# Performance work log

Measured on AMD Instinct MI355X. Metric: run time of the kernel, lower is better.

The kernel has to match this reference:

```python
import jax, jax.numpy as jnp
import numpy as np

S, B, D, H, K, M, MEM = 1024, 2, 1024, 16, 64, 4096, 1
T = (MEM + 1) * S  # key length = (mem_len+1)*seq_len


def setup_inputs() -> dict:
    key = jax.random.key(0)
    ks = jax.random.split(key, 16)

    def w(k, shape):  # N(0, 0.02) init as in the torch module
        return jax.random.normal(k, shape, dtype=jnp.float32) * 0.02

    x = jax.random.normal(ks[0], (S, B, D), dtype=jnp.float32)
    p = jax.random.normal(ks[1], (T, B, D), dtype=jnp.float32)
    memory = jax.random.normal(ks[2], (MEM * S, B, D), dtype=jnp.float32)
    u_bias = w(ks[3], (H, K))
    v_bias = w(ks[4], (H, K))
    # Transformer-XL causal mask: query s may attend to keys t <= mem_len*S + s
    t_idx = jnp.arange(T)[None, :]
    s_idx = jnp.arange(S)[:, None]
    mask = jnp.where(t_idx <= MEM * S + s_idx, 0.0, -1e9).astype(jnp.float32)[None]  # [1,S,T]
    return {
        "x": x, "p": p, "mask": mask, "memory": memory,
        "u_bias": u_bias, "v_bias": v_bias,
        "wq_w": w(ks[5], (H * K, D)), "wke_w": w(ks[6], (H * K, D)),
        "wkr_w": w(ks[7], (H * K, D)), "wv_w": w(ks[8], (H * K, D)),
        "wc_w": w(ks[9], (D, H * K)),
        "w1_w": w(ks[10], (M, D)), "w1_b": jnp.zeros((M,), jnp.float32),
        "w2_w": w(ks[11], (D, M)), "w2_b": jnp.zeros((D,), jnp.float32),
        "ln1_g": jnp.ones((D,), jnp.float32), "ln1_b": jnp.zeros((D,), jnp.float32),
        "ln2_g": jnp.ones((D,), jnp.float32), "ln2_b": jnp.zeros((D,), jnp.float32),
    }


def _layernorm(x, g, b, eps=1e-5):
    mu = jnp.mean(x, axis=-1, keepdims=True)
    var = jnp.mean(jnp.square(x - mu), axis=-1, keepdims=True)
    return (x - mu) / jnp.sqrt(var + eps) * g + b


def reference(x, p, mask, memory, u_bias, v_bias,
              wq_w, wke_w, wkr_w, wv_w, wc_w,
              w1_w, w1_b, w2_w, w2_b, ln1_g, ln1_b, ln2_g, ln2_b):
    s_len, b_sz, d = x.shape
    q = (x @ wq_w.T).reshape(s_len, b_sz, H, K)            # [S,B,H,K]
    x_mem = jnp.concatenate([memory, x], axis=0)           # [T,B,D]
    k_e = (x_mem @ wke_w.T).reshape(T, b_sz, H, K)         # content keys
    k_r = (p @ wkr_w.T).reshape(T, b_sz, H, K)             # relative-position keys
    v = (x_mem @ wv_w.T).reshape(T, b_sz, H, K)
    # AC: content score, BD: relative-position score (Transformer-XL)
    ac = jnp.einsum("sbhk,tbhk->bhst", q + u_bias, k_e)
    bd = jnp.einsum("sbhk,tbhk->bhst", q + v_bias, k_r)
    alpha = (ac + bd) / np.sqrt(K).astype(np.float32) + mask[:, None]  # [B,H,S,T]
    alpha = jax.nn.softmax(alpha, axis=-1)
    av = jnp.einsum("bhst,tbhk->sbhk", alpha, v).reshape(s_len, b_sz, H * K)
    u = av @ wc_w.T
    u = _layernorm(u + x, ln1_g, ln1_b)
    z = jax.nn.relu(u @ w1_w.T + w1_b) @ w2_w.T + w2_b
    z = _layernorm(z + u, ln2_g, ln2_b)
    return z
```

## Files before the change

kernel.cpp:

```cpp
#include <hip/hip_runtime.h>
#include <math.h>

#define S_LEN 1024
#define BATCH 2
#define DM 1024
#define NH 16
#define HD 64
#define FFN_DIM 4096
#define T_LEN 2048
#define RQ 2048
#define RT 4096
#define KROW 72
#define NPART 3
#define OPSTR 2097152L

typedef __attribute__((ext_vector_type(8))) short short8;
typedef __attribute__((ext_vector_type(4))) float f32x4;

__device__ __forceinline__ unsigned short f2bf(float f) {
    unsigned u = __builtin_bit_cast(unsigned, f);
    u += 0x7fffu + ((u >> 16) & 1u);
    return (unsigned short)(u >> 16);
}
__device__ __forceinline__ float bf2f(unsigned short s) { return __builtin_bit_cast(float, ((unsigned)s) << 16); }

#define GLD_LDS16(gptr, lptr)                                                                  \
    __builtin_amdgcn_global_load_lds((const __attribute__((address_space(1))) unsigned int*)(gptr), \
                                     (__attribute__((address_space(3))) unsigned int*)(lptr), 16, 0, 0)

__device__ __forceinline__ ushort4 cvt4(float4 v) {
    ushort4 o;
    o.x = f2bf(v.x); o.y = f2bf(v.y); o.z = f2bf(v.z); o.w = f2bf(v.w);
    return o;
}

__global__ void cast_all_kernel(const float* __restrict__ wq, const float* __restrict__ wke,
                                const float* __restrict__ wv, const float* __restrict__ wkr,
                                const float* __restrict__ wc, const float* __restrict__ w1,
                                const float* __restrict__ w2, const float* __restrict__ x,
                                const float* __restrict__ p, const float* __restrict__ mem,
                                unsigned short* __restrict__ wdst, unsigned short* __restrict__ xbf,
                                unsigned short* __restrict__ pbf, unsigned short* __restrict__ xm) {
    const long Q = 256 * 1024;
    const long W = 13 * Q;
    long i = (long)blockIdx.x * blockDim.x + threadIdx.x;
    if (i < W) {
        const float* src; long off;
        if      (i < 1 * Q) { src = wq;  off = 0; }
        else if (i < 2 * Q) { src = wke; off = 1 * Q; }
        else if (i < 3 * Q) { src = wv;  off = 2 * Q; }
        else if (i < 4 * Q) { src = wkr; off = 3 * Q; }
        else if (i < 5 * Q) { src = wc;  off = 4 * Q; }
        else if (i < 9 * Q) { src = w1;  off = 5 * Q; }
        else                { src = w2;  off = 9 * Q; }
        ((ushort4*)wdst)[i] = cvt4(((const float4*)src)[i - off]);
    } else if (i < W + 2 * Q) {
        long j = i - W;
        ((ushort4*)xbf)[j] = cvt4(((const float4*)x)[j]);
    } else if (i < W + 6 * Q) {
        long j = i - W - 2 * Q;
        ((ushort4*)pbf)[j] = cvt4(((const float4*)p)[j]);
    } else {
        long j = i - W - 6 * Q;
        float4 v = (j < 2 * Q) ? ((const float4*)mem)[j] : ((const float4*)x)[j - 2 * Q];
        ((ushort4*)xm)[j] = cvt4(v);
    }
}

#define BM 128
#define BN 128
#define BK 64


__launch_bounds__(256)
__global__ void proj_fused(const unsigned short* __restrict__ xbf, const unsigned short* __restrict__ xmbf,
                           const unsigned short* __restrict__ pbf, const unsigned short* __restrict__ wqb,
                           const unsigned short* __restrict__ wkevb, const unsigned short* __restrict__ wkrb,
                           unsigned short* __restrict__ qo, unsigned short* __restrict__ keo,
                           unsigned short* __restrict__ vTo, unsigned short* __restrict__ kro) {
    __shared__ __align__(16) short As[BM * BK];
    __shared__ __align__(16) short Bs[BN * BK];
    const int id = blockIdx.x;
    const unsigned short *A, *B;
    unsigned short *Yb, *Yv = nullptr;
    int bx, by;
    if (id < 128)      { A = xbf;  B = wqb;   Yb = qo;  bx = id & 7;   by = id >> 3; }
    else if (id < 640) { int t = id - 128; A = xmbf; B = wkevb; Yb = keo; Yv = vTo;
                         bx = t & 15; by = t >> 4; }
    else               { int t = id - 640; A = pbf;  B = wkrb;  Yb = kro;
                         bx = t & 7;  by = t >> 3; }
    const int tid = threadIdx.x;
    const int w = tid >> 6, lane = tid & 63;
    const int row0 = by * BM, col0 = bx * BN;
    const int wr = (w >> 1) * 64, wcn = (w & 1) * 64;
    f32x4 acc[4][4] = {};
    const int lrow = lane & 15, quad = lane >> 4;
    for (int k0 = 0; k0 < DM; k0 += BK) {
        __syncthreads();
#pragma unroll
        for (int i = 0; i < 4; ++i) {
            int c = i * 256 + tid;
            int row = c >> 3, ph = c & 7;
            int kl = (ph - row) & 7;
            GLD_LDS16(A + (long)(row0 + row) * DM + k0 + kl * 8, As + (i * 256 + w * 64) * 8);
            GLD_LDS16(B + (long)(col0 + row) * DM + k0 + kl * 8, Bs + (i * 256 + w * 64) * 8);
        }
        __syncthreads();
#pragma unroll
        for (int hh = 0; hh < 2; ++hh) {
            short8 a[4], b[4];
#pragma unroll
            for (int mi = 0; mi < 4; ++mi) {
                int r = wr + mi * 16 + lrow;
                int ph = (hh * 4 + quad + r) & 7;
                a[mi] = *(const short8*)&As[r * BK + ph * 8];
            }
#pragma unroll
            for (int ni = 0; ni < 4; ++ni) {
                int r = wcn + ni * 16 + lrow;
                int ph = (hh * 4 + quad + r) & 7;
                b[ni] = *(const short8*)&Bs[r * BK + ph * 8];
            }
#pragma unroll
            for (int mi = 0; mi < 4; ++mi)
#pragma unroll
                for (int ni = 0; ni < 4; ++ni)
                    acc[mi][ni] = __builtin_amdgcn_mfma_f32_16x16x32_bf16(a[mi], b[ni], acc[mi][ni], 0, 0, 0);
        }
    }
    const int mb = row0 + wr + quad * 4;
    const int nb = col0 + wcn + lrow;
    const bool isv = (Yv != nullptr) && (col0 >= 1024);
#pragma unroll
    for (int mi = 0; mi < 4; ++mi)
#pragma unroll
        for (int ni = 0; ni < 4; ++ni) {
            const int r = mb + mi * 16, cc = nb + ni * 16;
#pragma unroll
            for (int reg = 0; reg < 4; ++reg) {
                float val = acc[mi][ni][reg];
                const int rf = r + reg;
                if (isv) {
                    int c2 = cc - 1024;
                    int t = rf >> 1, b2 = rf & 1;
                    int h2 = c2 >> 6, d2 = c2 & 63;
                    Yv[((long)(b2 * NH + h2) * HD + d2) * T_LEN + t] = f2bf(val);
                } else {
                    Yb[(long)rf * DM + cc] = f2bf(val);
                }
            }
        }
}

__launch_bounds__(256)
__global__ void gemm_mfma(const unsigned short* __restrict__ A, const unsigned short* __restrict__ B,
                          const float* __restrict__ bias, float* __restrict__ Yf,
                          unsigned short* __restrict__ Yb, int Kd, int N, int relu,
                          int klen, long pstride) {
    __shared__ __align__(16) short As[BM * BK];
    __shared__ __align__(16) short Bs[BN * BK];
    const int tid = threadIdx.x;
    const int w = tid >> 6, lane = tid & 63;
    const int row0 = blockIdx.y * BM, col0 = blockIdx.x * BN;
    const int kbeg = blockIdx.z * klen;
    const int wr = (w >> 1) * 64, wcn = (w & 1) * 64;
    f32x4 acc[4][4] = {};
    const int lrow = lane & 15, quad = lane >> 4;
    for (int k0 = kbeg; k0 < kbeg + klen; k0 += BK) {
        __syncthreads();
#pragma unroll
        for (int i = 0; i < 4; ++i) {
            int c = i * 256 + tid;
            int row = c >> 3, ph = c & 7;
            int kl = (ph - row) & 7;
            GLD_LDS16(A + (long)(row0 + row) * Kd + k0 + kl * 8, As + (i * 256 + w * 64) * 8);
            GLD_LDS16(B + (long)(col0 + row) * Kd + k0 + kl * 8, Bs + (i * 256 + w * 64) * 8);
        }
        __syncthreads();
#pragma unroll
        for (int hh = 0; hh < 2; ++hh) {
            short8 a[4], b[4];
#pragma unroll
            for (int mi = 0; mi < 4; ++mi) {
                int r = wr + mi * 16 + lrow;
                int ph = (hh * 4 + quad + r) & 7;
                a[mi] = *(const short8*)&As[r * BK + ph * 8];
            }
#pragma unroll
            for (int ni = 0; ni < 4; ++ni) {
                int r = wcn + ni * 16 + lrow;
                int ph = (hh * 4 + quad + r) & 7;
                b[ni] = *(const short8*)&Bs[r * BK + ph * 8];
            }
#pragma unroll
            for (int mi = 0; mi < 4; ++mi)
#pragma unroll
                for (int ni = 0; ni < 4; ++ni)
                    acc[mi][ni] = __builtin_amdgcn_mfma_f32_16x16x32_bf16(a[mi], b[ni], acc[mi][ni], 0, 0, 0);
        }
    }
    const int mb = row0 + wr + quad * 4;
    const int nb = col0 + wcn + lrow;
    float* of = Yf ? Yf + (long)blockIdx.z * pstride : nullptr;
    float bb[4];
#pragma unroll
    for (int ni = 0; ni < 4; ++ni) bb[ni] = bias ? bias[nb + ni * 16] : 0.f;
#pragma unroll
    for (int mi = 0; mi < 4; ++mi)
#pragma unroll
        for (int ni = 0; ni < 4; ++ni) {
            const int r = mb + mi * 16, cc = nb + ni * 16;
#pragma unroll
            for (int reg = 0; reg < 4; ++reg) {
                float val = acc[mi][ni][reg] + bb[ni];
                if (relu) val = fmaxf(val, 0.f);
                if (Yb) Yb[(long)(r + reg) * N + cc] = f2bf(val);
                else    of[(long)(r + reg) * N + cc] = val;
            }
        }
}

__launch_bounds__(256)
__global__ void prep_kernel(const unsigned short* __restrict__ kr,
                            const float* __restrict__ ub, const float* __restrict__ vb,
                            unsigned short* __restrict__ ke_io, float* __restrict__ biasg) {
    const int r = blockIdx.x;
    const int tid = threadIdx.x;
    const int h = tid >> 4, seg = tid & 15;
    ushort4 keu = ((const ushort4*)(ke_io + (long)r * DM))[tid];
    ushort4 kru = ((const ushort4*)(kr + (long)r * DM))[tid];
    float ke0 = bf2f(keu.x), ke1 = bf2f(keu.y), ke2 = bf2f(keu.z), ke3 = bf2f(keu.w);
    float kr0 = bf2f(kru.x), kr1 = bf2f(kru.y), kr2 = bf2f(kru.z), kr3 = bf2f(kru.w);
    float4 u4 = ((const float4*)ub)[tid];
    float4 v4 = ((const float4*)vb)[tid];
    ushort4 s;
    s.x = f2bf((ke0 + kr0) * 0.125f); s.y = f2bf((ke1 + kr1) * 0.125f);
    s.z = f2bf((ke2 + kr2) * 0.125f); s.w = f2bf((ke3 + kr3) * 0.125f);
    ((ushort4*)(ke_io + (long)r * DM))[tid] = s;
    float part = u4.x * ke0 + u4.y * ke1 + u4.z * ke2 + u4.w * ke3
               + v4.x * kr0 + v4.y * kr1 + v4.z * kr2 + v4.w * kr3;
    part += __shfl_xor(part, 1);
    part += __shfl_xor(part, 2);
    part += __shfl_xor(part, 4);
    part += __shfl_xor(part, 8);
    if (seg == 0) {
        const int t = r >> 1, b = r & 1;
        biasg[(b * NH + h) * T_LEN + t] = part * 0.125f;
    }
}

__launch_bounds__(256)
__global__ void attn_mfma(const unsigned short* __restrict__ qg,
                          const unsigned short* __restrict__ ksum,
                          const unsigned short* __restrict__ vT,
                          const float* __restrict__ biasg,
                          float* __restrict__ Op01, float* __restrict__ Op2,
                          float2* __restrict__ mlout) {
    __shared__ __align__(16) unsigned short Ks[64 * KROW];
    __shared__ __align__(16) unsigned short Vs[64 * KROW];
    __shared__ __align__(16) unsigned short Ps[4][16 * KROW];
    const int bid = blockIdx.x;
    const int part = bid >> 9, rid = bid & 511;
    const int stile = rid & 15, h = (rid >> 4) & 15, b = rid >> 8;
    const int tid = threadIdx.x, w = tid >> 6, lane = tid & 63;
    const int L = lane & 15, quad = lane >> 4;
    const int qbase = stile * 64 + w * 16;
    short8 qf0, qf1;
    {
        const unsigned short* qp = qg + ((long)(qbase + L) * 2 + b) * DM + h * HD + quad * 8;
        qf0 = *(const short8*)(qp);
        qf1 = *(const short8*)(qp + 32);
    }
    f32x4 O[4] = {};
    float mrow[4] = {-1e30f, -1e30f, -1e30f, -1e30f};
    float lrow[4] = {0.f, 0.f, 0.f, 0.f};
    const int nch = 17 + stile;
    const float* bias_p = biasg + (long)(b * NH + h) * T_LEN;
    const unsigned short* ks_base = ksum + (long)b * DM + h * HD;
    const unsigned short* vt_base = vT + (long)(b * NH + h) * HD * T_LEN;
    const int c0 = tid, c1 = 256 + tid;
    const int row_a = c0 >> 3, seg_a = c0 & 7;
    const int row_b = c1 >> 3, seg_b = c1 & 7;
    uint4 pk0, pk1, pv0, pv1;
    float pb[4];
    {
        const int tf = part * 64;
        pk0 = *(const uint4*)(ks_base + (long)(tf + row_a) * 2 * DM + seg_a * 8);
        pk1 = *(const uint4*)(ks_base + (long)(tf + row_b) * 2 * DM + seg_b * 8);
        pv0 = *(const uint4*)(vt_base + (long)row_a * T_LEN + tf + seg_a * 8);
        pv1 = *(const uint4*)(vt_base + (long)row_b * T_LEN + tf + seg_b * 8);
#pragma unroll
        for (int kt = 0; kt < 4; ++kt) pb[kt] = bias_p[tf + kt * 16 + L];
    }
    for (int ch = part; ch < nch; ch += NPART) {
        const int t0 = ch * 64;
        __syncthreads();
        *(uint4*)&Ks[row_a * KROW + seg_a * 8] = pk0;
        *(uint4*)&Ks[row_b * KROW + seg_b * 8] = pk1;
        *(uint4*)&Vs[row_a * KROW + seg_a * 8] = pv0;
        *(uint4*)&Vs[row_b * KROW + seg_b * 8] = pv1;
        __syncthreads();
        const bool more = (ch + NPART < nch);
        float pbn[4];
        if (more) {
            const int t1 = t0 + NPART * 64;
            pk0 = *(const uint4*)(ks_base + (long)(t1 + row_a) * 2 * DM + seg_a * 8);
            pk1 = *(const uint4*)(ks_base + (long)(t1 + row_b) * 2 * DM + seg_b * 8);
            pv0 = *(const uint4*)(vt_base + (long)row_a * T_LEN + t1 + seg_a * 8);
            pv1 = *(const uint4*)(vt_base + (long)row_b * T_LEN + t1 + seg_b * 8);
#pragma unroll
            for (int kt = 0; kt < 4; ++kt) pbn[kt] = bias_p[t1 + kt * 16 + L];
        }
        f32x4 S[4] = {};
#pragma unroll
        for (int kt = 0; kt < 4; ++kt) {
            short8 kb0 = *(const short8*)&Ks[(kt * 16 + L) * KROW + quad * 8];
            short8 kb1 = *(const short8*)&Ks[(kt * 16 + L) * KROW + 32 + quad * 8];
            S[kt] = __builtin_amdgcn_mfma_f32_16x16x32_bf16(qf0, kb0, S[kt], 0, 0, 0);
            S[kt] = __builtin_amdgcn_mfma_f32_16x16x32_bf16(qf1, kb1, S[kt], 0, 0, 0);
        }
        float sc[4][4];
        float cm[4] = {-1e30f, -1e30f, -1e30f, -1e30f};
        if (ch != nch - 1) {
#pragma unroll
            for (int kt = 0; kt < 4; ++kt)
#pragma unroll
                for (int reg = 0; reg < 4; ++reg) {
                    float v = S[kt][reg] + pb[kt];
                    sc[kt][reg] = v;
                    cm[reg] = fmaxf(cm[reg], v);
                }
        } else {
#pragma unroll
            for (int kt = 0; kt < 4; ++kt)
#pragma unroll
                for (int reg = 0; reg < 4; ++reg) {
                    float v = S[kt][reg] + pb[kt];
                    if (t0 + kt * 16 + L > 1024 + qbase + quad * 4 + reg) v = -1e30f;
                    sc[kt][reg] = v;
                    cm[reg] = fmaxf(cm[reg], v);
                }
        }
#pragma unroll
        for (int off = 1; off < 16; off <<= 1)
#pragma unroll
            for (int reg = 0; reg < 4; ++reg) cm[reg] = fmaxf(cm[reg], __shfl_xor(cm[reg], off));
        float cf[4];
#pragma unroll
        for (int reg = 0; reg < 4; ++reg) {
            float mn = fmaxf(mrow[reg], cm[reg]);
            cf[reg] = __expf(mrow[reg] - mn);
            mrow[reg] = mn;
            lrow[reg] *= cf[reg];
        }
        float rs[4] = {0.f, 0.f, 0.f, 0.f};
#pragma unroll
        for (int kt = 0; kt < 4; ++kt)
#pragma unroll
            for (int reg = 0; reg < 4; ++reg) {
                float pv = __expf(sc[kt][reg] - mrow[reg]);
                rs[reg] += pv;
                Ps[w][(quad * 4 + reg) * KROW + kt * 16 + L] = f2bf(pv);
            }
#pragma unroll
        for (int off = 1; off < 16; off <<= 1)
#pragma unroll
            for (int reg = 0; reg < 4; ++reg) rs[reg] += __shfl_xor(rs[reg], off);
#pragma unroll
        for (int reg = 0; reg < 4; ++reg) lrow[reg] += rs[reg];
#pragma unroll
        for (int dt = 0; dt < 4; ++dt)
#pragma unroll
            for (int reg = 0; reg < 4; ++reg) O[dt][reg] *= cf[reg];
        short8 pa0 = *(const short8*)&Ps[w][L * KROW + quad * 8];
        short8 pa1 = *(const short8*)&Ps[w][L * KROW + 32 + quad * 8];
#pragma unroll
        for (int dt = 0; dt < 4; ++dt) {
            short8 vb0 = *(const short8*)&Vs[(dt * 16 + L) * KROW + quad * 8];
            short8 vb1 = *(const short8*)&Vs[(dt * 16 + L) * KROW + 32 + quad * 8];
            O[dt] = __builtin_amdgcn_mfma_f32_16x16x32_bf16(pa0, vb0, O[dt], 0, 0, 0);
            O[dt] = __builtin_amdgcn_mfma_f32_16x16x32_bf16(pa1, vb1, O[dt], 0, 0, 0);
        }
        if (more) {
#pragma unroll
            for (int kt = 0; kt < 4; ++kt) pb[kt] = pbn[kt];
        }
    }
    float* ob = (part < 2) ? Op01 + (long)part * OPSTR : Op2;
    const long rbase = ((long)b * NH + h) * S_LEN;
#pragma unroll
    for (int reg = 0; reg < 4; ++reg) {
        const int s = qbase + quad * 4 + reg;
        float* op = ob + (rbase + s) * 64;
#pragma unroll
        for (int dt = 0; dt < 4; ++dt) op[dt * 16 + L] = O[dt][reg];
        if (L == 0) mlout[(long)part * 32768 + rbase + s] = make_float2(mrow[reg], lrow[reg]);
    }
}

__launch_bounds__(256)
__global__ void attn_combine(const float* __restrict__ Op01, const float* __restrict__ Op2,
                             const float2* __restrict__ ml,
                             unsigned short* __restrict__ avout) {
    const int i = blockIdx.x * 256 + threadIdx.x;
    const int d4 = i & 15;
    const int row = i >> 4;
    const int s = row & 1023;
    const int bh = row >> 10;
    const int b = bh >> 4, h = bh & 15;
    float2 m0 = ml[row], m1 = ml[row + 32768], m2 = ml[row + 65536];
    float m = fmaxf(fmaxf(m0.x, m1.x), m2.x);
    float a0 = __expf(m0.x - m), a1 = __expf(m1.x - m), a2 = __expf(m2.x - m);
    float inv = 1.f / (a0 * m0.y + a1 * m1.y + a2 * m2.y);
    a0 *= inv; a1 *= inv; a2 *= inv;
    float4 o0 = ((const float4*)Op01)[(long)row * 16 + d4];
    float4 o1 = ((const float4*)Op01)[((long)row + 32768) * 16 + d4];
    float4 o2 = ((const float4*)Op2)[(long)row * 16 + d4];
    float4 o;
    o.x = a0 * o0.x + a1 * o1.x + a2 * o2.x;
    o.y = a0 * o0.y + a1 * o1.y + a2 * o2.y;
    o.z = a0 * o0.z + a1 * o1.z + a2 * o2.z;
    o.w = a0 * o0.w + a1 * o1.w + a2 * o2.w;
    *(ushort4*)(avout + ((long)s * 2 + b) * DM + h * HD + d4 * 4) = cvt4(o);
}

__launch_bounds__(256)
__global__ void ln_kernel(const float* __restrict__ a0, const float* __restrict__ a1,
                          const float* __restrict__ cb, const float* __restrict__ r,
                          const float* __restrict__ g, const float* __restrict__ be,
                          float* __restrict__ out, unsigned short* __restrict__ outb) {
    const int row = blockIdx.x;
    const int tid = threadIdx.x;
    float4 xa = ((const float4*)(a0 + (long)row * DM))[tid];
    if (a1) {
        float4 x1 = ((const float4*)(a1 + (long)row * DM))[tid];
        xa.x += x1.x; xa.y += x1.y; xa.z += x1.z; xa.w += x1.w;
    }
    if (cb) {
        float4 c4 = ((const float4*)cb)[tid];
        xa.x += c4.x; xa.y += c4.y; xa.z += c4.z; xa.w += c4.w;
    }
    float4 xr = ((const float4*)(r + (long)row * DM))[tid];
    float4 x = make_float4(xa.x + xr.x, xa.y + xr.y, xa.z + xr.z, xa.w + xr.w);
    float s1 = x.x + x.y + x.z + x.w;
    float s2 = x.x * x.x + x.y * x.y + x.z * x.z + x.w * x.w;
#pragma unroll
    for (int off = 32; off > 0; off >>= 1) {
        s1 += __shfl_down(s1, off);
        s2 += __shfl_down(s2, off);
    }
    __shared__ float w1s[4], w2s[4];
    const int wid = tid >> 6;
    if ((tid & 63) == 0) { w1s[wid] = s1; w2s[wid] = s2; }
    __syncthreads();
    float S1 = w1s[0] + w1s[1] + w1s[2] + w1s[3];
    float S2 = w2s[0] + w2s[1] + w2s[2] + w2s[3];
    float mu = S1 * (1.f / 1024.f);
    float var = S2 * (1.f / 1024.f) - mu * mu;
    float rstd = rsqrtf(var + 1e-5f);
    float4 gv = ((const float4*)g)[tid];
    float4 bv = ((const float4*)be)[tid];
    float4 o;
    o.x = (x.x - mu) * rstd * gv.x + bv.x;
    o.y = (x.y - mu) * rstd * gv.y + bv.y;
    o.z = (x.z - mu) * rstd * gv.z + bv.z;
    o.w = (x.w - mu) * rstd * gv.w + bv.w;
    ((float4*)(out + (long)row * DM))[tid] = o;
    if (outb) ((ushort4*)(outb + (long)row * DM))[tid] = cvt4(o);
}

extern "C" void kernel_launch(void* const* d_in, const int* in_sizes, int n_in,
                              void* d_out, int out_size, void* d_ws, size_t ws_size,
                              hipStream_t stream) {
    (void)in_sizes; (void)n_in; (void)out_size; (void)ws_size;
    const float* x    = (const float*)d_in[0];
    const float* p    = (const float*)d_in[1];
    const float* mem  = (const float*)d_in[3];
    const float* ub   = (const float*)d_in[4];
    const float* vb   = (const float*)d_in[5];
    const float* wq   = (const float*)d_in[6];
    const float* wke  = (const float*)d_in[7];
    const float* wkr  = (const float*)d_in[8];
    const float* wv   = (const float*)d_in[9];
    const float* wc   = (const float*)d_in[10];
    const float* w1   = (const float*)d_in[11];
    const float* w1b  = (const float*)d_in[12];
    const float* w2   = (const float*)d_in[13];
    const float* w2b  = (const float*)d_in[14];
    const float* ln1g = (const float*)d_in[15];
    const float* ln1b = (const float*)d_in[16];
    const float* ln2g = (const float*)d_in[17];
    const float* ln2b = (const float*)d_in[18];
    float* out = (float*)d_out;
    float* wsf = (float*)d_ws;
    unsigned short* ws16 = (unsigned short*)d_ws;

    const long HLF = 512 * 1024;
    const long M16 = 1024 * 1024;
    unsigned short* wq_bf   = ws16 + 0 * M16;
    unsigned short* wkev_bf = ws16 + 1 * M16;
    unsigned short* wkr_bf  = ws16 + 3 * M16;
    unsigned short* wc_bf   = ws16 + 4 * M16;
    unsigned short* w1_bf   = ws16 + 5 * M16;
    unsigned short* w2_bf   = ws16 + 9 * M16;
    unsigned short* x_bf   = (unsigned short*)(wsf + 13 * HLF);
    unsigned short* xm_bf  = (unsigned short*)(wsf + 15 * HLF);
    unsigned short* p_bf   = (unsigned short*)(wsf + 19 * HLF);
    unsigned short* q_bf   = (unsigned short*)(wsf + 23 * HLF);
    unsigned short* ke_bf  = (unsigned short*)(wsf + 25 * HLF);
    unsigned short* kr_bf  = (unsigned short*)(wsf + 29 * HLF);
    unsigned short* vT_bf  = (unsigned short*)(wsf + 33 * HLF);
    float* abias           = wsf + 37 * HLF;
    float2* mlpart         = (float2*)(wsf + 13 * HLF);
    float* Op01            = wsf + 15 * HLF;
    float* Op2             = wsf + 29 * HLF;
    unsigned short* avb_bf = (unsigned short*)(wsf + 33 * HLF);
    float* t1p             = wsf + 15 * HLF;
    float* u               = wsf + 25 * HLF;
    unsigned short* u_bf   = (unsigned short*)(wsf + 23 * HLF);
    unsigned short* z1_bf  = (unsigned short*)(wsf + 13 * HLF);
    float* t2p             = wsf + 29 * HLF;
    const long PSTR = (long)2048 * 1024;

    cast_all_kernel<<<23552, 256, 0, stream>>>(wq, wke, wv, wkr, wc, w1, w2, x, p, mem,
                                               ws16, x_bf, p_bf, xm_bf);
    proj_fused<<<896, 256, 0, stream>>>(x_bf, xm_bf, p_bf, wq_bf, wkev_bf, wkr_bf,
                                        q_bf, ke_bf, vT_bf, kr_bf);
    prep_kernel<<<RT, 256, 0, stream>>>(kr_bf, ub, vb, ke_bf, abias);
    attn_mfma<<<512 * NPART, 256, 0, stream>>>(q_bf, ke_bf, vT_bf, abias, Op01, Op2, mlpart);
    attn_combine<<<2048, 256, 0, stream>>>(Op01, Op2, mlpart, avb_bf);
    gemm_mfma<<<dim3(8, 16, 2), 256, 0, stream>>>(avb_bf, wc_bf, nullptr, t1p, nullptr,
                                                  DM, DM, 0, 512, PSTR);
    ln_kernel<<<RQ, 256, 0, stream>>>(t1p, t1p + PSTR, nullptr, x, ln1g, ln1b, u, u_bf);
    gemm_mfma<<<dim3(32, 16, 1), 256, 0, stream>>>(u_bf, w1_bf, w1b, nullptr, z1_bf,
                                                   DM, FFN_DIM, 1, DM, 0);
    gemm_mfma<<<dim3(8, 16, 2), 256, 0, stream>>>(z1_bf, w2_bf, nullptr, t2p, nullptr,
                                                  FFN_DIM, DM, 0, 2048, PSTR);
    ln_kernel<<<RQ, 256, 0, stream>>>(t2p, t2p + PSTR, w2b, u, ln2g, ln2b, out, nullptr);
}
```

Baseline: 381.8 us.

## Remap blocks across XCDs, halve projection K-tile, add MFMA priority hints

Block indices in the projection, attention and GEMM kernels are permuted so that consecutive logical tiles land on the same XCD (the index is taken modulo 8 and strided), which should improve L2 reuse of shared operand panels. The GEMM launches become 1D grids whose tile coordinates are decoded in-kernel. The fused projection kernel's K-tile drops from 64 to 32 with a new LDS swizzle, halving its LDS footprint to allow more resident blocks, at the cost of twice as many barriers. The attention kernel wraps its MFMA sections in s_setprio so the matrix work gets issue priority over other waves.

```diff
diff --git a/kernel.cpp b/kernel.cpp
--- a/kernel.cpp
+++ b/kernel.cpp
@@ -7,9 +7,9 @@
 #define NH 16
 #define HD 64
 #define FFN_DIM 4096
-#define T_LEN 2048
 #define RQ 2048
 #define RT 4096
+#define T_LEN 2048
 #define KROW 72
 #define NPART 3
 #define OPSTR 2097152L
@@ -69,8 +69,8 @@
 
 #define BM 128
 #define BN 128
-#define BK 64
-
+#define GBK 64
+#define PBK 32
 
 __launch_bounds__(256)
 __global__ void proj_fused(const unsigned short* __restrict__ xbf, const unsigned short* __restrict__ xmbf,
@@ -78,9 +78,10 @@
                            const unsigned short* __restrict__ wkevb, const unsigned short* __restrict__ wkrb,
                            unsigned short* __restrict__ qo, unsigned short* __restrict__ keo,
                            unsigned short* __restrict__ vTo, unsigned short* __restrict__ kro) {
-    __shared__ __align__(16) short As[BM * BK];
-    __shared__ __align__(16) short Bs[BN * BK];
-    const int id = blockIdx.x;
+    __shared__ __align__(16) short As[BM * PBK];
+    __shared__ __align__(16) short Bs[BN * PBK];
+    const int id0 = blockIdx.x;
+    const int id = (id0 & 7) * 112 + (id0 >> 3);
     const unsigned short *A, *B;
     unsigned short *Yb, *Yv = nullptr;
     int bx, by;
@@ -95,38 +96,35 @@
     const int wr = (w >> 1) * 64, wcn = (w & 1) * 64;
     f32x4 acc[4][4] = {};
     const int lrow = lane & 15, quad = lane >> 4;
-    for (int k0 = 0; k0 < DM; k0 += BK) {
+    for (int k0 = 0; k0 < DM; k0 += PBK) {
         __syncthreads();
 #pragma unroll
-        for (int i = 0; i < 4; ++i) {
-            int c = i * 256 + tid;
-            int row = c >> 3, ph = c & 7;
-            int kl = (ph - row) & 7;
-            GLD_LDS16(A + (long)(row0 + row) * DM + k0 + kl * 8, As + (i * 256 + w * 64) * 8);
-            GLD_LDS16(B + (long)(col0 + row) * DM + k0 + kl * 8, Bs + (i * 256 + w * 64) * 8);
+        for (int i = 0; i < 2; ++i) {
+            int c = w * 128 + i * 64 + lane;
+            int row = c >> 2, kg = c & 3;
+            int kl = (kg - (row >> 1)) & 3;
+            GLD_LDS16(A + (long)(row0 + row) * DM + k0 + kl * 8, As + (w * 128 + i * 64) * 8);
+            GLD_LDS16(B + (long)(col0 + row) * DM + k0 + kl * 8, Bs + (w * 128 + i * 64) * 8);
         }
         __syncthreads();
-#pragma unroll
-        for (int hh = 0; hh < 2; ++hh) {
-            short8 a[4], b[4];
-#pragma unroll
-            for (int mi = 0; mi < 4; ++mi) {
-                int r = wr + mi * 16 + lrow;
-                int ph = (hh * 4 + quad + r) & 7;
-                a[mi] = *(const short8*)&As[r * BK + ph * 8];
-            }
-#pragma unroll
-            for (int ni = 0; ni < 4; ++ni) {
-                int r = wcn + ni * 16 + lrow;
-                int ph = (hh * 4 + quad + r) & 7;
-                b[ni] = *(const short8*)&Bs[r * BK + ph * 8];
-            }
-#pragma unroll
-            for (int mi = 0; mi < 4; ++mi)
-#pragma unroll
-                for (int ni = 0; ni < 4; ++ni)
-                    acc[mi][ni] = __builtin_amdgcn_mfma_f32_16x16x32_bf16(a[mi], b[ni], acc[mi][ni], 0, 0, 0);
-        }
+        short8 a[4], b[4];
+#pragma unroll
+        for (int mi = 0; mi < 4; ++mi) {
+            int r = wr + mi * 16 + lrow;
+            int ph = (quad + (r >> 1)) & 3;
+            a[mi] = *(const short8*)&As[r * PBK + ph * 8];
+        }
+#pragma unroll
+        for (int ni = 0; ni < 4; ++ni) {
+            int r = wcn + ni * 16 + lrow;
+            int ph = (quad + (r >> 1)) & 3;
+            b[ni] = *(const short8*)&Bs[r * PBK + ph * 8];
+        }
+#pragma unroll
+        for (int mi = 0; mi < 4; ++mi)
+#pragma unroll
+            for (int ni = 0; ni < 4; ++ni)
+                acc[mi][ni] = __builtin_amdgcn_mfma_f32_16x16x32_bf16(a[mi], b[ni], acc[mi][ni], 0, 0, 0);
     }
     const int mb = row0 + wr + quad * 4;
     const int nb = col0 + wcn + lrow;
@@ -157,16 +155,23 @@
                           const float* __restrict__ bias, float* __restrict__ Yf,
                           unsigned short* __restrict__ Yb, int Kd, int N, int relu,
                           int klen, long pstride) {
-    __shared__ __align__(16) short As[BM * BK];
-    __shared__ __align__(16) short Bs[BN * BK];
+    __shared__ __align__(16) short As[BM * GBK];
+    __shared__ __align__(16) short Bs[BN * GBK];
+    const int nbx = N >> 7;
+    const int cpx = gridDim.x >> 3;
+    const int bid = ((blockIdx.x & 7) * cpx) + (blockIdx.x >> 3);
+    const int per_z = nbx << 4;
+    const int z = bid / per_z;
+    const int r2 = bid - z * per_z;
+    const int by = r2 / nbx, bx = r2 - by * nbx;
     const int tid = threadIdx.x;
     const int w = tid >> 6, lane = tid & 63;
-    const int row0 = blockIdx.y * BM, col0 = blockIdx.x * BN;
-    const int kbeg = blockIdx.z * klen;
+    const int row0 = by * BM, col0 = bx * BN;
+    const int kbeg = z * klen;
     const int wr = (w >> 1) * 64, wcn = (w & 1) * 64;
     f32x4 acc[4][4] = {};
     const int lrow = lane & 15, quad = lane >> 4;
-    for (int k0 = kbeg; k0 < kbeg + klen; k0 += BK) {
+    for (int k0 = kbeg; k0 < kbeg + klen; k0 += GBK) {
         __syncthreads();
 #pragma unroll
         for (int i = 0; i < 4; ++i) {
@@ -184,13 +189,13 @@
             for (int mi = 0; mi < 4; ++mi) {
                 int r = wr + mi * 16 + lrow;
                 int ph = (hh * 4 + quad + r) & 7;
-                a[mi] = *(const short8*)&As[r * BK + ph * 8];
+                a[mi] = *(const short8*)&As[r * GBK + ph * 8];
             }
 #pragma unroll
             for (int ni = 0; ni < 4; ++ni) {
                 int r = wcn + ni * 16 + lrow;
                 int ph = (hh * 4 + quad + r) & 7;
-                b[ni] = *(const short8*)&Bs[r * BK + ph * 8];
+                b[ni] = *(const short8*)&Bs[r * GBK + ph * 8];
             }
 #pragma unroll
             for (int mi = 0; mi < 4; ++mi)
@@ -201,7 +206,7 @@
     }
     const int mb = row0 + wr + quad * 4;
     const int nb = col0 + wcn + lrow;
-    float* of = Yf ? Yf + (long)blockIdx.z * pstride : nullptr;
+    float* of = Yf ? Yf + (long)z * pstride : nullptr;
     float bb[4];
 #pragma unroll
     for (int ni = 0; ni < 4; ++ni) bb[ni] = bias ? bias[nb + ni * 16] : 0.f;
@@ -259,7 +264,8 @@
     __shared__ __align__(16) unsigned short Ks[64 * KROW];
     __shared__ __align__(16) unsigned short Vs[64 * KROW];
     __shared__ __align__(16) unsigned short Ps[4][16 * KROW];
-    const int bid = blockIdx.x;
+    const int bid0 = blockIdx.x;
+    const int bid = (bid0 & 7) * 192 + (bid0 >> 3);
     const int part = bid >> 9, rid = bid & 511;
     const int stile = rid & 15, h = (rid >> 4) & 15, b = rid >> 8;
     const int tid = threadIdx.x, w = tid >> 6, lane = tid & 63;
@@ -312,6 +318,7 @@
             for (int kt = 0; kt < 4; ++kt) pbn[kt] = bias_p[t1 + kt * 16 + L];
         }
         f32x4 S[4] = {};
+        __builtin_amdgcn_s_setprio(1);
 #pragma unroll
         for (int kt = 0; kt < 4; ++kt) {
             short8 kb0 = *(const short8*)&Ks[(kt * 16 + L) * KROW + quad * 8];
@@ -319,6 +326,7 @@
             S[kt] = __builtin_amdgcn_mfma_f32_16x16x32_bf16(qf0, kb0, S[kt], 0, 0, 0);
             S[kt] = __builtin_amdgcn_mfma_f32_16x16x32_bf16(qf1, kb1, S[kt], 0, 0, 0);
         }
+        __builtin_amdgcn_s_setprio(0);
         float sc[4][4];
         float cm[4] = {-1e30f, -1e30f, -1e30f, -1e30f};
         if (ch != nch - 1) {
@@ -374,6 +382,7 @@
             for (int reg = 0; reg < 4; ++reg) O[dt][reg] *= cf[reg];
         short8 pa0 = *(const short8*)&Ps[w][L * KROW + quad * 8];
         short8 pa1 = *(const short8*)&Ps[w][L * KROW + 32 + quad * 8];
+        __builtin_amdgcn_s_setprio(1);
 #pragma unroll
         for (int dt = 0; dt < 4; ++dt) {
             short8 vb0 = *(const short8*)&Vs[(dt * 16 + L) * KROW + quad * 8];
@@ -381,6 +390,7 @@
             O[dt] = __builtin_amdgcn_mfma_f32_16x16x32_bf16(pa0, vb0, O[dt], 0, 0, 0);
             O[dt] = __builtin_amdgcn_mfma_f32_16x16x32_bf16(pa1, vb1, O[dt], 0, 0, 0);
         }
+        __builtin_amdgcn_s_setprio(0);
         if (more) {
 #pragma unroll
             for (int kt = 0; kt < 4; ++kt) pb[kt] = pbn[kt];
@@ -529,12 +539,12 @@
     prep_kernel<<<RT, 256, 0, stream>>>(kr_bf, ub, vb, ke_bf, abias);
     attn_mfma<<<512 * NPART, 256, 0, stream>>>(q_bf, ke_bf, vT_bf, abias, Op01, Op2, mlpart);
     attn_combine<<<2048, 256, 0, stream>>>(Op01, Op2, mlpart, avb_bf);
-    gemm_mfma<<<dim3(8, 16, 2), 256, 0, stream>>>(avb_bf, wc_bf, nullptr, t1p, nullptr,
-                                                  DM, DM, 0, 512, PSTR);
+    gemm_mfma<<<256, 256, 0, stream>>>(avb_bf, wc_bf, nullptr, t1p, nullptr,
+                                       DM, DM, 0, 512, PSTR);
     ln_kernel<<<RQ, 256, 0, stream>>>(t1p, t1p + PSTR, nullptr, x, ln1g, ln1b, u, u_bf);
-    gemm_mfma<<<dim3(32, 16, 1), 256, 0, stream>>>(u_bf, w1_bf, w1b, nullptr, z1_bf,
-                                                   DM, FFN_DIM, 1, DM, 0);
-    gemm_mfma<<<dim3(8, 16, 2), 256, 0, stream>>>(z1_bf, w2_bf, nullptr, t2p, nullptr,
-                                                  FFN_DIM, DM, 0, 2048, PSTR);
+    gemm_mfma<<<512, 256, 0, stream>>>(u_bf, w1_bf, w1b, nullptr, z1_bf,
+                                       DM, FFN_DIM, 1, DM, 0);
+    gemm_mfma<<<256, 256, 0, stream>>>(z1_bf, w2_bf, nullptr, t2p, nullptr,
+                                       FFN_DIM, DM, 0, 2048, PSTR);
     ln_kernel<<<RQ, 256, 0, stream>>>(t2p, t2p + PSTR, w2b, u, ln2g, ln2b, out, nullptr);
 }
```

After: 377.9 us. No clear change (-1.0%).
